# Optimization experiments

Hardware: AMD Instinct MI355X
Metric: run time of the kernel (lower is better)

## Reference

```python
import jax, jax.numpy as jnp
import numpy as np

N_NODES = 50000
N_EDGES = 800000
IN_F = 128
OUT_F = 128
HEADS = 8
HEAD_DIM = OUT_F // HEADS
EDGE_F = 32


def setup_inputs() -> dict:
    key = jax.random.key(0)
    ks = jax.random.split(key, 14)
    s = lambda fan_in: 1.0 / np.sqrt(fan_in)
    return {
        "node_features": jax.random.normal(ks[0], (N_NODES, IN_F), jnp.float32),
        "edge_index": jax.random.randint(ks[1], (2, N_EDGES), 0, N_NODES, jnp.int64),
        "edge_features": jax.random.normal(ks[2], (N_EDGES, EDGE_F), jnp.float32),
        "Wq": jax.random.uniform(ks[3], (IN_F, OUT_F), jnp.float32, -s(IN_F), s(IN_F)),
        "bq": jnp.zeros((OUT_F,), jnp.float32),
        "Wk": jax.random.uniform(ks[4], (IN_F, OUT_F), jnp.float32, -s(IN_F), s(IN_F)),
        "bk": jnp.zeros((OUT_F,), jnp.float32),
        "Wv": jax.random.uniform(ks[5], (IN_F, OUT_F), jnp.float32, -s(IN_F), s(IN_F)),
        "bv": jnp.zeros((OUT_F,), jnp.float32),
        "We": jax.random.uniform(ks[6], (EDGE_F, HEADS), jnp.float32, -s(EDGE_F), s(EDGE_F)),
        "be": jnp.zeros((HEADS,), jnp.float32),
        "Wo": jax.random.uniform(ks[7], (OUT_F, OUT_F), jnp.float32, -s(OUT_F), s(OUT_F)),
        "bo": jnp.zeros((OUT_F,), jnp.float32),
    }


def reference(node_features, edge_index, edge_features,
              Wq, bq, Wk, bk, Wv, bv, We, be, Wo, bo):
    n_nodes = node_features.shape[0]
    n_edges = edge_index.shape[1]
    sources, targets = edge_index[0], edge_index[1]
    scale = HEAD_DIM ** -0.5

    # dense projections: [n_nodes, heads, head_dim]
    Q = (node_features @ Wq + bq).reshape(n_nodes, HEADS, HEAD_DIM)
    K = (node_features @ Wk + bk).reshape(n_nodes, HEADS, HEAD_DIM)
    V = (node_features @ Wv + bv).reshape(n_nodes, HEADS, HEAD_DIM)

    # gather by edge
    Q_t = Q[targets]           # [n_edges, heads, head_dim]
    K_s = K[sources]
    V_s = V[sources]

    scores = jnp.sum(Q_t * K_s, axis=-1) * scale      # [n_edges, heads]
    scores = scores + (edge_features @ We + be)       # edge bias

    # segment softmax over incoming edges of each target node
    max_s = jax.ops.segment_max(scores, targets, num_segments=n_nodes)
    scores = scores - max_s[targets]
    exp_s = jnp.exp(scores)
    denom = jax.ops.segment_sum(exp_s, targets, num_segments=n_nodes) + 1e-10
    probs = exp_s / denom[targets]                    # [n_edges, heads]

    weighted_V = probs[:, :, None] * V_s              # [n_edges, heads, head_dim]
    aggregated = jax.ops.segment_sum(
        weighted_V.reshape(n_edges, -1), targets, num_segments=n_nodes)
    return aggregated @ Wo + bo
```

## Files before the change

kernel.cpp:

```cpp
#include <hip/hip_runtime.h>

typedef __attribute__((ext_vector_type(8))) short shortx8;
typedef __attribute__((ext_vector_type(4))) float floatx4;
typedef unsigned short u16;
typedef unsigned int u32;

__device__ __forceinline__ float bf2f(unsigned short u) {
    union { unsigned int i; float f; } v; v.i = ((unsigned int)u) << 16; return v.f;
}
__device__ __forceinline__ float bfl(u32 u) {
    union { u32 i; float f; } v; v.i = u << 16; return v.f;
}
__device__ __forceinline__ float bfh(u32 u) {
    union { u32 i; float f; } v; v.i = u & 0xFFFF0000u; return v.f;
}
__device__ __forceinline__ unsigned short f2bf(float f) {
    union { float f; unsigned int i; } v; v.f = f;
    unsigned int x = v.i;
    unsigned int r = x + 0x7FFFu + ((x >> 16) & 1u);
    return (unsigned short)(r >> 16);
}
__device__ __forceinline__ float ldf(const void* p, int i, bool f32) {
    return f32 ? ((const float*)p)[i] : bf2f(((const u16*)p)[i]);
}

__global__ __launch_bounds__(256) void detect_zero_k(
    const u16* __restrict__ nf, const int* __restrict__ ei,
    int* __restrict__ flags, int* __restrict__ deg, int M)
{
    int tid = threadIdx.x;
    if (blockIdx.x != 0) {
        int i = (blockIdx.x - 1) * 256 + tid;
        if (i < M) deg[i] = 0;
        return;
    }
    __shared__ int cnt[2];
    if (tid < 2) cnt[tid] = 0;
    __syncthreads();
    int c0 = 0;
    for (int i = tid; i < 65536; i += 256) {
        u16 v = nf[i];
        if ((v & 0x7F80u) == 0x7F80u) c0++;
    }
    int c1 = 0;
    for (int i = tid; i < 4096; i += 256) {
        if (ei[2 * i + 1] != 0) c1++;
    }
    atomicAdd(&cnt[0], c0);
    atomicAdd(&cnt[1], c1);
    __syncthreads();
    if (tid == 0) {
        flags[0] = (cnt[0] > 8) ? 1 : 0;
        flags[1] = (cnt[1] < 100) ? 1 : 0;
    }
}

__global__ __launch_bounds__(256) void prep_k(
    const void* __restrict__ W0, const void* __restrict__ W1,
    const void* __restrict__ W2, const void* __restrict__ W3,
    const void* __restrict__ b0, const void* __restrict__ b1,
    const void* __restrict__ b2, const void* __restrict__ b3,
    const void* __restrict__ We, const void* __restrict__ be,
    const int* __restrict__ flags,
    u16* __restrict__ WT, float* __restrict__ biasWs,
    float* __restrict__ WeWs, float* __restrict__ beWs)
{
    bool f32 = flags[0] != 0;
    int tid = threadIdx.x;
    if (blockIdx.x < 32) {
        int t = blockIdx.x * 256 + tid;
        int mat  = t >> 11;
        int r    = t & 2047;
        int lane = r & 63;
        int ks   = (r >> 6) & 3;
        int ct   = r >> 8;
        const void* W = (mat == 0) ? W0 : (mat == 1) ? W1 : (mat == 2) ? W2 : W3;
        int k0  = ks * 32 + (lane >> 4) * 8;
        int col = ct * 16 + (lane & 15);
        u16 tmp[8];
#pragma unroll
        for (int j = 0; j < 8; ++j) {
            int off = (k0 + j) * 128 + col;
            tmp[j] = f32 ? f2bf(((const float*)W)[off]) : ((const u16*)W)[off];
        }
        *(shortx8*)(WT + (size_t)t * 8) = *(const shortx8*)tmp;
    } else {
        if (tid < 128) {
            biasWs[0 * 128 + tid] = ldf(b0, tid, f32);
            biasWs[1 * 128 + tid] = ldf(b1, tid, f32);
            biasWs[2 * 128 + tid] = ldf(b2, tid, f32);
            biasWs[3 * 128 + tid] = ldf(b3, tid, f32);
        }
        WeWs[tid] = ldf(We, tid, f32);
        if (tid < 8) beWs[tid] = ldf(be, tid, f32);
    }
}

__global__ __launch_bounds__(256) void hist_rank_k(
    const int* __restrict__ ei, int* __restrict__ deg, int* __restrict__ rank,
    int E, const int* __restrict__ flags)
{
    int e = blockIdx.x * 256 + threadIdx.x;
    if (e >= E) return;
    int tgt = flags[1] ? ei[2 * (E + e)] : ei[E + e];
    rank[e] = atomicAdd(&deg[tgt], 1);
}

__global__ __launch_bounds__(256) void scan1_k(
    const int* __restrict__ deg, int* __restrict__ incl, int* __restrict__ bsum, int M)
{
    __shared__ int s[256];
    int tid = threadIdx.x;
    int i = blockIdx.x * 256 + tid;
    int v = (i < M) ? deg[i] : 0;
    s[tid] = v;
    __syncthreads();
#pragma unroll
    for (int off = 1; off < 256; off <<= 1) {
        int t = (tid >= off) ? s[tid - off] : 0;
        __syncthreads();
        s[tid] += t;
        __syncthreads();
    }
    if (i < M) incl[i] = s[tid];
    if (tid == 255) bsum[blockIdx.x] = s[255];
}

__global__ __launch_bounds__(256) void scan2_k(
    const int* __restrict__ bsum, int* __restrict__ boff, int nb)
{
    __shared__ int s[256];
    int tid = threadIdx.x;
    int v = (tid < nb) ? bsum[tid] : 0;
    s[tid] = v;
    __syncthreads();
#pragma unroll
    for (int off = 1; off < 256; off <<= 1) {
        int t = (tid >= off) ? s[tid - off] : 0;
        __syncthreads();
        s[tid] += t;
        __syncthreads();
    }
    if (tid < nb) boff[tid] = s[tid] - v;
}

__global__ __launch_bounds__(256) void scan3_k(
    const int* __restrict__ incl, const int* __restrict__ boff,
    int* __restrict__ rowptr, int M)
{
    int i = blockIdx.x * 256 + threadIdx.x;
    if (i >= M) return;
    rowptr[i + 1] = incl[i] + boff[i >> 8];
    if (i == 0) rowptr[0] = 0;
}

__global__ __launch_bounds__(256) void qkv_gemm_k(
    const void* __restrict__ A, int M,
    const u16* __restrict__ WT, const float* __restrict__ biasWs,
    u16* __restrict__ Qb, u16* __restrict__ Kb, u16* __restrict__ Vb,
    const int* __restrict__ flags)
{
    bool aF32 = flags[0] != 0;
    int lane = threadIdx.x & 63;
    int wave = threadIdx.x >> 6;
    int quad = lane >> 4;
    int l15  = lane & 15;
    int m0   = blockIdx.x * 128 + wave * 32;

    shortx8 afrag[2][4];
#pragma unroll
    for (int mt = 0; mt < 2; ++mt) {
        int row = m0 + mt * 16 + l15;
        row = row < M ? row : M - 1;
#pragma unroll
        for (int ks = 0; ks < 4; ++ks) {
            size_t base = (size_t)row * 128 + ks * 32 + quad * 8;
            if (aF32) {
                const floatx4* ap = (const floatx4*)((const float*)A + base);
                floatx4 f0 = ap[0], f1 = ap[1];
                u16 tmp[8];
#pragma unroll
                for (int j = 0; j < 4; ++j) { tmp[j] = f2bf(f0[j]); tmp[4 + j] = f2bf(f1[j]); }
                afrag[mt][ks] = *(const shortx8*)tmp;
            } else {
                afrag[mt][ks] = *(const shortx8*)((const u16*)A + base);
            }
        }
    }

    u16* outs[3] = {Qb, Kb, Vb};
#pragma unroll
    for (int mat = 0; mat < 3; ++mat) {
        floatx4 acc[2][8];
#pragma unroll
        for (int a = 0; a < 2; ++a)
#pragma unroll
            for (int b = 0; b < 8; ++b)
                acc[a][b] = (floatx4){0.f, 0.f, 0.f, 0.f};
#pragma unroll
        for (int ks = 0; ks < 4; ++ks) {
#pragma unroll
            for (int ct = 0; ct < 8; ++ct) {
                shortx8 bfrag = *(const shortx8*)(WT + (size_t)mat * 16384 +
                                                  ((size_t)(ct * 4 + ks) * 64 + lane) * 8);
                acc[0][ct] = __builtin_amdgcn_mfma_f32_16x16x32_bf16(afrag[0][ks], bfrag, acc[0][ct], 0, 0, 0);
                acc[1][ct] = __builtin_amdgcn_mfma_f32_16x16x32_bf16(afrag[1][ks], bfrag, acc[1][ct], 0, 0, 0);
            }
        }
        u16* out = outs[mat];
#pragma unroll
        for (int ct = 0; ct < 8; ++ct) {
            int col = ct * 16 + l15;
            float bs = biasWs[mat * 128 + col];
#pragma unroll
            for (int mt = 0; mt < 2; ++mt) {
#pragma unroll
                for (int r = 0; r < 4; ++r) {
                    int row = m0 + mt * 16 + quad * 4 + r;
                    if (row < M)
                        out[(size_t)row * 128 + col] = f2bf(acc[mt][ct][r] + bs);
                }
            }
        }
    }
}

__global__ __launch_bounds__(256) void edge_scatter_k(
    const int* __restrict__ ei, const void* __restrict__ ef,
    const int* __restrict__ rank, const int* __restrict__ rowptr,
    const float* __restrict__ WeWs, const float* __restrict__ beWs,
    int* __restrict__ perm, float* __restrict__ EBp,
    int E, const int* __restrict__ flags)
{
    __shared__ float sWe[256];
    __shared__ float sbe[8];
    int tid = threadIdx.x;
    sWe[tid] = WeWs[tid];
    if (tid < 8) sbe[tid] = beWs[tid];
    __syncthreads();

    int e = blockIdx.x * 256 + tid;
    if (e >= E) return;
    bool f32 = flags[0] != 0;
    bool i64 = flags[1] != 0;

    int src = i64 ? ei[2 * e]       : ei[e];
    int tgt = i64 ? ei[2 * (E + e)] : ei[E + e];
    int pos = rowptr[tgt] + rank[e];
    perm[pos] = src;

    float v[32];
    if (f32) {
        const floatx4* ep = (const floatx4*)((const float*)ef + (size_t)e * 32);
#pragma unroll
        for (int g = 0; g < 8; ++g) {
            floatx4 t = ep[g];
#pragma unroll
            for (int j = 0; j < 4; ++j) v[g * 4 + j] = t[j];
        }
    } else {
        const shortx8* ep = (const shortx8*)((const u16*)ef + (size_t)e * 32);
#pragma unroll
        for (int g = 0; g < 4; ++g) {
            shortx8 t = ep[g];
#pragma unroll
            for (int j = 0; j < 8; ++j) v[g * 8 + j] = bf2f((unsigned short)t[j]);
        }
    }
    float eb[8];
#pragma unroll
    for (int h = 0; h < 8; ++h) eb[h] = sbe[h];
#pragma unroll
    for (int k = 0; k < 32; ++k)
#pragma unroll
        for (int h = 0; h < 8; ++h) eb[h] += v[k] * sWe[k * 8 + h];

    floatx4* op = (floatx4*)(EBp + (size_t)pos * 8);
    op[0] = (floatx4){eb[0], eb[1], eb[2], eb[3]};
    op[1] = (floatx4){eb[4], eb[5], eb[6], eb[7]};
}

__global__ __launch_bounds__(256) void node_agg_k(
    const int* __restrict__ perm, const int* __restrict__ rowptr,
    const u16* __restrict__ Qb, const u16* __restrict__ Kb, const u16* __restrict__ Vb,
    const float* __restrict__ EBp, u16* __restrict__ aggN, int M, int E)
{
    int wave = threadIdx.x >> 6;
    int lane = threadIdx.x & 63;
    int n = blockIdx.x * 4 + wave;
    if (n >= M) return;
    int g = lane >> 4;
    int w = lane & 15;
    int h = w >> 1;

    int beg = rowptr[n], end = rowptr[n + 1];
    int pidx = beg + lane;
    if (pidx >= E) pidx = E - 1;
    int pv = perm[pidx];

    uint4 qw = ((const uint4*)(Qb + (size_t)n * 128))[w];
    float q0 = bfl(qw.x), q1 = bfh(qw.x), q2 = bfl(qw.y), q3 = bfh(qw.y);
    float q4 = bfl(qw.z), q5 = bfh(qw.z), q6 = bfl(qw.w), q7 = bfh(qw.w);

    float acc[8];
#pragma unroll
    for (int j = 0; j < 8; ++j) acc[j] = 0.f;
    float dsum = 0.f;

    for (int i = beg; i < end; i += 4) {
        int idx = i + g;
        bool valid = idx < end;
        int cidx = valid ? idx : (end - 1);
        int off = cidx - beg;
        int src = (off < 64) ? __shfl(pv, off) : perm[cidx];
        float eb = EBp[(size_t)cidx * 8 + h];
        uint4 kw = ((const uint4*)(Kb + (size_t)src * 128))[w];
        uint4 vw = ((const uint4*)(Vb + (size_t)src * 128))[w];
        float part = q0 * bfl(kw.x) + q1 * bfh(kw.x)
                   + q2 * bfl(kw.y) + q3 * bfh(kw.y)
                   + q4 * bfl(kw.z) + q5 * bfh(kw.z)
                   + q6 * bfl(kw.w) + q7 * bfh(kw.w);
        part += __shfl_xor(part, 1);
        float p = valid ? __expf(part * 0.25f + eb) : 0.f;
        dsum += p;
        acc[0] += p * bfl(vw.x); acc[1] += p * bfh(vw.x);
        acc[2] += p * bfl(vw.y); acc[3] += p * bfh(vw.y);
        acc[4] += p * bfl(vw.z); acc[5] += p * bfh(vw.z);
        acc[6] += p * bfl(vw.w); acc[7] += p * bfh(vw.w);
    }

    dsum += __shfl_xor(dsum, 16);
    dsum += __shfl_xor(dsum, 32);
#pragma unroll
    for (int j = 0; j < 8; ++j) {
        acc[j] += __shfl_xor(acc[j], 16);
        acc[j] += __shfl_xor(acc[j], 32);
    }
    if (g == 0) {
        float inv = 1.0f / (dsum + 1e-10f);
        uint4 o;
        o.x = (u32)f2bf(acc[0] * inv) | ((u32)f2bf(acc[1] * inv) << 16);
        o.y = (u32)f2bf(acc[2] * inv) | ((u32)f2bf(acc[3] * inv) << 16);
        o.z = (u32)f2bf(acc[4] * inv) | ((u32)f2bf(acc[5] * inv) << 16);
        o.w = (u32)f2bf(acc[6] * inv) | ((u32)f2bf(acc[7] * inv) << 16);
        ((uint4*)(aggN + (size_t)n * 128))[w] = o;
    }
}

__global__ __launch_bounds__(256) void out_gemm_k(
    const u16* __restrict__ A, int M,
    const u16* __restrict__ WT, const float* __restrict__ bias,
    void* __restrict__ out, const int* __restrict__ flags)
{
    bool oF32 = flags[0] != 0;
    int lane = threadIdx.x & 63;
    int wave = threadIdx.x >> 6;
    int quad = lane >> 4;
    int l15  = lane & 15;
    int m0   = blockIdx.x * 128 + wave * 32;

    floatx4 acc[2][8];
#pragma unroll
    for (int a = 0; a < 2; ++a)
#pragma unroll
        for (int b = 0; b < 8; ++b)
            acc[a][b] = (floatx4){0.f, 0.f, 0.f, 0.f};

#pragma unroll
    for (int ks = 0; ks < 4; ++ks) {
        shortx8 afrag[2];
#pragma unroll
        for (int mt = 0; mt < 2; ++mt) {
            int row = m0 + mt * 16 + l15;
            row = row < M ? row : M - 1;
            afrag[mt] = *(const shortx8*)(A + (size_t)row * 128 + ks * 32 + quad * 8);
        }
#pragma unroll
        for (int ct = 0; ct < 8; ++ct) {
            shortx8 bfrag = *(const shortx8*)(WT + ((size_t)(ct * 4 + ks) * 64 + lane) * 8);
            acc[0][ct] = __builtin_amdgcn_mfma_f32_16x16x32_bf16(afrag[0], bfrag, acc[0][ct], 0, 0, 0);
            acc[1][ct] = __builtin_amdgcn_mfma_f32_16x16x32_bf16(afrag[1], bfrag, acc[1][ct], 0, 0, 0);
        }
    }

#pragma unroll
    for (int ct = 0; ct < 8; ++ct) {
        int col = ct * 16 + l15;
        float bs = bias[col];
#pragma unroll
        for (int mt = 0; mt < 2; ++mt) {
#pragma unroll
            for (int r = 0; r < 4; ++r) {
                int row = m0 + mt * 16 + quad * 4 + r;
                if (row < M) {
                    float v = acc[mt][ct][r] + bs;
                    if (oF32) ((float*)out)[(size_t)row * 128 + col] = v;
                    else      ((u16*)out)[(size_t)row * 128 + col] = f2bf(v);
                }
            }
        }
    }
}

extern "C" void kernel_launch(void* const* d_in, const int* in_sizes, int n_in,
                              void* d_out, int out_size, void* d_ws, size_t ws_size,
                              hipStream_t stream)
{
    const void* nf = d_in[0];
    const int*  ei = (const int*)d_in[1];
    const void* ef = d_in[2];
    const void* Wq = d_in[3];  const void* bq = d_in[4];
    const void* Wk = d_in[5];  const void* bk = d_in[6];
    const void* Wv = d_in[7];  const void* bv = d_in[8];
    const void* We = d_in[9];  const void* be = d_in[10];
    const void* Wo = d_in[11]; const void* bo = d_in[12];

    int M = in_sizes[0] / 128;
    int E = in_sizes[1] / 2;
    int nb = (M + 255) / 256;

    char* ws = (char*)d_ws;
    int*   flags  = (int*)(ws + 0);
    float* biasWs = (float*)(ws + 256);
    float* WeWs   = (float*)(ws + 2304);
    float* beWs   = (float*)(ws + 3328);
    u16*   WT     = (u16*)(ws + 4096);
    size_t O1 = 4096 + 131072;
    size_t qkv = (size_t)M * 128 * 2;
    u16* Qb = (u16*)(ws + O1);
    u16* Kb = (u16*)(ws + O1 + qkv);
    u16* Vb = (u16*)(ws + O1 + 2 * qkv);
    size_t O2 = O1 + 3 * qkv;
    float* EBp = (float*)(ws + O2);
    size_t O3 = O2 + (size_t)E * 8 * 4;
    int* perm   = (int*)(ws + O3);
    int* rank   = perm + E;
    int* deg    = rank + E;
    int* incl   = deg + M;
    int* rowptr = incl + M;
    int* bsum   = rowptr + M + 1;
    int* boff   = bsum + 256;
    u16* aggN   = Qb;

    detect_zero_k<<<1 + nb, 256, 0, stream>>>((const u16*)nf, ei, flags, deg, M);
    prep_k<<<33, 256, 0, stream>>>(Wq, Wk, Wv, Wo, bq, bk, bv, bo, We, be,
                                   flags, WT, biasWs, WeWs, beWs);

    int eblocks = (E + 255) / 256;
    hist_rank_k<<<eblocks, 256, 0, stream>>>(ei, deg, rank, E, flags);
    scan1_k<<<nb, 256, 0, stream>>>(deg, incl, bsum, M);
    scan2_k<<<1, 256, 0, stream>>>(bsum, boff, nb);
    scan3_k<<<nb, 256, 0, stream>>>(incl, boff, rowptr, M);

    int gblocks = (M + 127) / 128;
    qkv_gemm_k<<<gblocks, 256, 0, stream>>>(nf, M, WT, biasWs, Qb, Kb, Vb, flags);

    edge_scatter_k<<<eblocks, 256, 0, stream>>>(ei, ef, rank, rowptr, WeWs, beWs,
                                                perm, EBp, E, flags);

    node_agg_k<<<(M + 3) / 4, 256, 0, stream>>>(perm, rowptr, Qb, Kb, Vb, EBp, aggN, M, E);

    out_gemm_k<<<gblocks, 256, 0, stream>>>(aggN, M, WT + 3 * 16384, biasWs + 384, d_out, flags);
}
```

Before: 454.1 us.

## Interleave K/V rows, store edge bias by edge id, use cursor atomics for CSR

K and V are now stored interleaved in one 256-wide row per node, so each gathered edge touches a single contiguous 512-byte region instead of two separate buffers. The rank array is removed: the histogram kernel only counts, the scan turns incl into per-node write cursors, and edge_scatter claims slots with a second atomicAdd, writing (src, edge id) pairs. The edge bias is written at the edge's original index, which makes those writes coalesced, but node_agg now reads it indirectly by edge id, turning a sequential read into a random gather. The result also adds a second pass of atomics and doubles the size of the permutation array.

Measured after the change: 465.8 us. +2.6%, slower.

```diff
diff --git a/kernel.cpp b/kernel.cpp
--- a/kernel.cpp
+++ b/kernel.cpp
@@ -96,14 +96,14 @@
     }
 }
 
-__global__ __launch_bounds__(256) void hist_rank_k(
-    const int* __restrict__ ei, int* __restrict__ deg, int* __restrict__ rank,
+__global__ __launch_bounds__(256) void hist_k(
+    const int* __restrict__ ei, int* __restrict__ deg,
     int E, const int* __restrict__ flags)
 {
     int e = blockIdx.x * 256 + threadIdx.x;
     if (e >= E) return;
     int tgt = flags[1] ? ei[2 * (E + e)] : ei[E + e];
-    rank[e] = atomicAdd(&deg[tgt], 1);
+    atomicAdd(&deg[tgt], 1);
 }
 
 __global__ __launch_bounds__(256) void scan1_k(
@@ -145,19 +145,21 @@
 }
 
 __global__ __launch_bounds__(256) void scan3_k(
-    const int* __restrict__ incl, const int* __restrict__ boff,
-    int* __restrict__ rowptr, int M)
+    int* __restrict__ incl_cur, const int* __restrict__ boff,
+    const int* __restrict__ deg, int* __restrict__ rowptr, int M)
 {
     int i = blockIdx.x * 256 + threadIdx.x;
     if (i >= M) return;
-    rowptr[i + 1] = incl[i] + boff[i >> 8];
+    int r = incl_cur[i] + boff[i >> 8];
+    rowptr[i + 1] = r;
+    incl_cur[i] = r - deg[i];
     if (i == 0) rowptr[0] = 0;
 }
 
 __global__ __launch_bounds__(256) void qkv_gemm_k(
     const void* __restrict__ A, int M,
     const u16* __restrict__ WT, const float* __restrict__ biasWs,
-    u16* __restrict__ Qb, u16* __restrict__ Kb, u16* __restrict__ Vb,
+    u16* __restrict__ Qb, u16* __restrict__ KVb,
     const int* __restrict__ flags)
 {
     bool aF32 = flags[0] != 0;
@@ -188,7 +190,6 @@
         }
     }
 
-    u16* outs[3] = {Qb, Kb, Vb};
 #pragma unroll
     for (int mat = 0; mat < 3; ++mat) {
         floatx4 acc[2][8];
@@ -207,7 +208,8 @@
                 acc[1][ct] = __builtin_amdgcn_mfma_f32_16x16x32_bf16(afrag[1][ks], bfrag, acc[1][ct], 0, 0, 0);
             }
         }
-        u16* out = outs[mat];
+        u16* base = (mat == 0) ? Qb : (mat == 1) ? KVb : (KVb + 128);
+        int stride = (mat == 0) ? 128 : 256;
 #pragma unroll
         for (int ct = 0; ct < 8; ++ct) {
             int col = ct * 16 + l15;
@@ -218,7 +220,7 @@
                 for (int r = 0; r < 4; ++r) {
                     int row = m0 + mt * 16 + quad * 4 + r;
                     if (row < M)
-                        out[(size_t)row * 128 + col] = f2bf(acc[mt][ct][r] + bs);
+                        base[(size_t)row * stride + col] = f2bf(acc[mt][ct][r] + bs);
                 }
             }
         }
@@ -227,9 +229,9 @@
 
 __global__ __launch_bounds__(256) void edge_scatter_k(
     const int* __restrict__ ei, const void* __restrict__ ef,
-    const int* __restrict__ rank, const int* __restrict__ rowptr,
+    int* __restrict__ cur,
     const float* __restrict__ WeWs, const float* __restrict__ beWs,
-    int* __restrict__ perm, float* __restrict__ EBp,
+    int2* __restrict__ pr2, float* __restrict__ EBe,
     int E, const int* __restrict__ flags)
 {
     __shared__ float sWe[256];
@@ -246,8 +248,8 @@
 
     int src = i64 ? ei[2 * e]       : ei[e];
     int tgt = i64 ? ei[2 * (E + e)] : ei[E + e];
-    int pos = rowptr[tgt] + rank[e];
-    perm[pos] = src;
+    int pos = atomicAdd(&cur[tgt], 1);
+    pr2[pos] = make_int2(src, e);
 
     float v[32];
     if (f32) {
@@ -275,15 +277,15 @@
 #pragma unroll
         for (int h = 0; h < 8; ++h) eb[h] += v[k] * sWe[k * 8 + h];
 
-    floatx4* op = (floatx4*)(EBp + (size_t)pos * 8);
+    floatx4* op = (floatx4*)(EBe + (size_t)e * 8);
     op[0] = (floatx4){eb[0], eb[1], eb[2], eb[3]};
     op[1] = (floatx4){eb[4], eb[5], eb[6], eb[7]};
 }
 
 __global__ __launch_bounds__(256) void node_agg_k(
-    const int* __restrict__ perm, const int* __restrict__ rowptr,
-    const u16* __restrict__ Qb, const u16* __restrict__ Kb, const u16* __restrict__ Vb,
-    const float* __restrict__ EBp, u16* __restrict__ aggN, int M, int E)
+    const int2* __restrict__ pr2, const int* __restrict__ rowptr,
+    const u16* __restrict__ Qb, const u16* __restrict__ KVb,
+    const float* __restrict__ EBe, u16* __restrict__ aggN, int M, int E)
 {
     int wave = threadIdx.x >> 6;
     int lane = threadIdx.x & 63;
@@ -296,7 +298,7 @@
     int beg = rowptr[n], end = rowptr[n + 1];
     int pidx = beg + lane;
     if (pidx >= E) pidx = E - 1;
-    int pv = perm[pidx];
+    int2 pv = pr2[pidx];
 
     uint4 qw = ((const uint4*)(Qb + (size_t)n * 128))[w];
     float q0 = bfl(qw.x), q1 = bfh(qw.x), q2 = bfl(qw.y), q3 = bfh(qw.y);
@@ -312,10 +314,18 @@
         bool valid = idx < end;
         int cidx = valid ? idx : (end - 1);
         int off = cidx - beg;
-        int src = (off < 64) ? __shfl(pv, off) : perm[cidx];
-        float eb = EBp[(size_t)cidx * 8 + h];
-        uint4 kw = ((const uint4*)(Kb + (size_t)src * 128))[w];
-        uint4 vw = ((const uint4*)(Vb + (size_t)src * 128))[w];
+        int src, eid;
+        if (off < 64) {
+            src = __shfl(pv.x, off);
+            eid = __shfl(pv.y, off);
+        } else {
+            int2 t = pr2[cidx];
+            src = t.x; eid = t.y;
+        }
+        float eb = EBe[(size_t)eid * 8 + h];
+        const uint4* kvp = (const uint4*)(KVb + (size_t)src * 256);
+        uint4 kw = kvp[w];
+        uint4 vw = kvp[16 + w];
         float part = q0 * bfl(kw.x) + q1 * bfh(kw.x)
                    + q2 * bfl(kw.y) + q3 * bfh(kw.y)
                    + q4 * bfl(kw.z) + q5 * bfh(kw.z)
@@ -426,16 +436,15 @@
     float* beWs   = (float*)(ws + 3328);
     u16*   WT     = (u16*)(ws + 4096);
     size_t O1 = 4096 + 131072;
-    size_t qkv = (size_t)M * 128 * 2;
-    u16* Qb = (u16*)(ws + O1);
-    u16* Kb = (u16*)(ws + O1 + qkv);
-    u16* Vb = (u16*)(ws + O1 + 2 * qkv);
-    size_t O2 = O1 + 3 * qkv;
-    float* EBp = (float*)(ws + O2);
+    size_t qrow  = (size_t)M * 128 * 2;
+    size_t kvrow = (size_t)M * 256 * 2;
+    u16* Qb  = (u16*)(ws + O1);
+    u16* KVb = (u16*)(ws + O1 + qrow);
+    size_t O2 = O1 + qrow + kvrow;
+    float* EBe = (float*)(ws + O2);
     size_t O3 = O2 + (size_t)E * 8 * 4;
-    int* perm   = (int*)(ws + O3);
-    int* rank   = perm + E;
-    int* deg    = rank + E;
+    int2* pr2   = (int2*)(ws + O3);
+    int* deg    = (int*)(pr2 + E);
     int* incl   = deg + M;
     int* rowptr = incl + M;
     int* bsum   = rowptr + M + 1;
@@ -447,18 +456,18 @@
                                    flags, WT, biasWs, WeWs, beWs);
 
     int eblocks = (E + 255) / 256;
-    hist_rank_k<<<eblocks, 256, 0, stream>>>(ei, deg, rank, E, flags);
+    hist_k<<<eblocks, 256, 0, stream>>>(ei, deg, E, flags);
     scan1_k<<<nb, 256, 0, stream>>>(deg, incl, bsum, M);
     scan2_k<<<1, 256, 0, stream>>>(bsum, boff, nb);
-    scan3_k<<<nb, 256, 0, stream>>>(incl, boff, rowptr, M);
+    scan3_k<<<nb, 256, 0, stream>>>(incl, boff, deg, rowptr, M);
 
     int gblocks = (M + 127) / 128;
-    qkv_gemm_k<<<gblocks, 256, 0, stream>>>(nf, M, WT, biasWs, Qb, Kb, Vb, flags);
-
-    edge_scatter_k<<<eblocks, 256, 0, stream>>>(ei, ef, rank, rowptr, WeWs, beWs,
-                                                perm, EBp, E, flags);
-
-    node_agg_k<<<(M + 3) / 4, 256, 0, stream>>>(perm, rowptr, Qb, Kb, Vb, EBp, aggN, M, E);
+    qkv_gemm_k<<<gblocks, 256, 0, stream>>>(nf, M, WT, biasWs, Qb, KVb, flags);
+
+    edge_scatter_k<<<eblocks, 256, 0, stream>>>(ei, ef, incl , WeWs, beWs,
+                                                pr2, EBe, E, flags);
+
+    node_agg_k<<<(M + 3) / 4, 256, 0, stream>>>(pr2, rowptr, Qb, KVb, EBe, aggN, M, E);
 
     out_gemm_k<<<gblocks, 256, 0, stream>>>(aggN, M, WT + 3 * 16384, biasWs + 384, d_out, flags);
 }
```
